# Kernel optimization log

Hardware: AMD Instinct MI355X
Metric: run time of the kernel (lower is better)

The kernel has to match this reference:

```python
import jax, jax.numpy as jnp
import numpy as np

D_NODE, C, N_HEAD = 64, 8, 8
LN_EPS = 1e-5
MASK_EPS = 1e-10
INF = 1e9


def setup_inputs() -> dict:
    key = jax.random.key(0)
    ks = jax.random.split(key, 12)
    B, S, R, D = 1, 2048, 384, D_NODE
    HC = N_HEAD * C
    M_raw = jax.random.normal(ks[0], (B, S, R, D), dtype=jnp.float32)
    M_mask = (jax.random.uniform(ks[1], (B, S, R)) > 0.1).astype(jnp.float32)
    sc = 1.0 / np.sqrt(D)
    return {
        "M_raw": M_raw,
        "M_mask": M_mask,
        "ln_g": jnp.ones((D,), jnp.float32),
        "ln_b": jnp.zeros((D,), jnp.float32),
        "Wq": jax.random.normal(ks[2], (D, HC), jnp.float32) * sc,
        "Wk": jax.random.normal(ks[3], (D, C), jnp.float32) * sc,
        "Wv": jax.random.normal(ks[4], (D, C), jnp.float32) * sc,
        "Wg": jax.random.normal(ks[5], (D, HC), jnp.float32) * sc,
        "bg": jnp.ones((HC,), jnp.float32),  # gating bias init to 1
        "Wo": jax.random.normal(ks[6], (HC, D), jnp.float32) * sc,
        "bo": jnp.zeros((D,), jnp.float32),
    }


def reference(M_raw, M_mask, ln_g, ln_b, Wq, Wk, Wv, Wg, bg, Wo, bo):
    # [B,S,R,D] -> [B,R,S,D]: attend over the sequence (column) axis per residue
    M = jnp.swapaxes(M_raw, -2, -3)
    mask = jnp.swapaxes(M_mask, -1, -2)  # [B,R,S]
    # LayerNorm over d_node
    mu = jnp.mean(M, axis=-1, keepdims=True)
    var = jnp.mean(jnp.square(M - mu), axis=-1, keepdims=True)
    M = (M - mu) * jax.lax.rsqrt(var + LN_EPS) * ln_g + ln_b
    # mean-pooled query over masked sequence positions -> [B,R,D]
    q_avg = jnp.sum(M * mask[..., None], axis=-2) / (jnp.sum(mask, axis=-1)[..., None] + MASK_EPS)
    q = (q_avg @ Wq).reshape(q_avg.shape[:-1] + (N_HEAD, C)) * (C ** -0.5)  # [B,R,H,c]
    k = M @ Wk  # [B,R,S,c] (shared across heads)
    v = M @ Wv  # [B,R,S,c]
    bias = (INF * (mask - 1.0))[..., None, :]  # [B,R,1,S]
    logits = jnp.einsum("brhc,brsc->brhs", q, k) + bias
    w = jax.nn.softmax(logits, axis=-1)
    o = jnp.einsum("brhs,brsc->brhc", w, v)  # [B,R,H,c]
    # per-position sigmoid gate broadcast against the single pooled output
    g = jax.nn.sigmoid(M @ Wg + bg).reshape(M.shape[:-1] + (N_HEAD, C))  # [B,R,S,H,c]
    go = (g * o[..., None, :, :]).reshape(M.shape[:-1] + (N_HEAD * C,))  # [B,R,S,H*c]
    out = go @ Wo + bo  # [B,R,S,D]
    return M_raw + jnp.swapaxes(out, -2, -3)
```

## Files before the change

### kernel.cpp

```cpp
#include <hip/hip_runtime.h>
#include <stdint.h>


#define DEV __device__ __forceinline__

typedef __attribute__((ext_vector_type(8))) short short8;
typedef __attribute__((ext_vector_type(4))) float floatx4;

static constexpr int S_DIM = 2048;
static constexpr int R_DIM = 384;

static constexpr size_t KV_OFF    = 0;
static constexpr size_t STATS_OFF = 25165824;
static constexpr size_t QPART_OFF = 31457280;
static constexpr size_t O_OFF     = 32342016;

DEV float bf2f(uint32_t u) { union { uint32_t i; float f; } c; c.i = u << 16; return c.f; }
DEV uint16_t f2bf(float f) {
  union { float f; uint32_t i; } c; c.f = f;
  return (uint16_t)((c.i + 0x7FFFu + ((c.i >> 16) & 1u)) >> 16);
}
DEV void unpack8(uint4 w, float* x) {
  x[0] = bf2f(w.x & 0xffff); x[1] = bf2f(w.x >> 16);
  x[2] = bf2f(w.y & 0xffff); x[3] = bf2f(w.y >> 16);
  x[4] = bf2f(w.z & 0xffff); x[5] = bf2f(w.z >> 16);
  x[6] = bf2f(w.w & 0xffff); x[7] = bf2f(w.w >> 16);
}

__global__ __launch_bounds__(256) void k1_ln_kv(
    const float* __restrict__ M, const float* __restrict__ mask,
    const float* __restrict__ lng, const float* __restrict__ lnb,
    const float* __restrict__ Wk, const float* __restrict__ Wv,
    uint16_t* __restrict__ kv, float* __restrict__ stats, float* __restrict__ qpart)
{
  __shared__ uint16_t mlnL[256 * 72];
  __shared__ uint16_t WkvT[16 * 72];
  __shared__ uint16_t kvL[256 * 16];
  __shared__ float redq[4][64];
  __shared__ float redc[4];

  const int tid = threadIdx.x;
  const int r = blockIdx.y;
  const int s_base = blockIdx.x * 256;
  const int w = tid >> 6, lane = tid & 63;
  const int g = lane >> 4, c4 = lane & 15;

#pragma unroll
  for (int i = 0; i < 4; ++i) {
    const int e = i * 256 + tid;
    const int n = e >> 6, d = e & 63;
    const float val = (n < 8) ? Wk[d * 8 + n] : Wv[d * 8 + (n - 8)];
    WkvT[n * 72 + d] = f2bf(val);
  }
  const float4 lngv = ((const float4*)lng)[c4];
  const float4 lnbv = ((const float4*)lnb)[c4];

  float qacc[4] = {0.f, 0.f, 0.f, 0.f};
  float cacc = 0.f;

#pragma unroll
  for (int j = 0; j < 16; ++j) {
    const int row_local = w * 64 + j * 4 + g;
    const int s = s_base + row_local;
    const size_t grow = (size_t)s * R_DIM + r;
    const float4 x = ((const float4*)(M + grow * 64))[c4];
    float sum = x.x + x.y + x.z + x.w;
    float ss = x.x * x.x + x.y * x.y + x.z * x.z + x.w * x.w;
#pragma unroll
    for (int off = 1; off < 16; off <<= 1) {
      sum += __shfl_xor(sum, off, 64);
      ss  += __shfl_xor(ss, off, 64);
    }
    const float mu = sum * (1.f / 64.f);
    const float var = ss * (1.f / 64.f) - mu * mu;
    const float rstd = 1.f / sqrtf(var + 1e-5f);
    if (c4 == 0) ((float2*)stats)[(size_t)r * S_DIM + s] = make_float2(mu, rstd);
    float y[4];
    y[0] = (x.x - mu) * rstd * lngv.x + lnbv.x;
    y[1] = (x.y - mu) * rstd * lngv.y + lnbv.y;
    y[2] = (x.z - mu) * rstd * lngv.z + lnbv.z;
    y[3] = (x.w - mu) * rstd * lngv.w + lnbv.w;
    uint2 p;
    p.x = (uint32_t)f2bf(y[0]) | ((uint32_t)f2bf(y[1]) << 16);
    p.y = (uint32_t)f2bf(y[2]) | ((uint32_t)f2bf(y[3]) << 16);
    *(uint2*)&mlnL[row_local * 72 + c4 * 4] = p;
    const float mval = mask[grow];
    qacc[0] += mval * y[0]; qacc[1] += mval * y[1];
    qacc[2] += mval * y[2]; qacc[3] += mval * y[3];
    cacc += mval;
  }

#pragma unroll
  for (int off = 16; off < 64; off <<= 1) {
#pragma unroll
    for (int i = 0; i < 4; ++i) qacc[i] += __shfl_xor(qacc[i], off, 64);
  }
#pragma unroll
  for (int off = 1; off < 64; off <<= 1) cacc += __shfl_xor(cacc, off, 64);
  if (lane < 16) {
    float4 qv = make_float4(qacc[0], qacc[1], qacc[2], qacc[3]);
    *(float4*)&redq[w][c4 * 4] = qv;
  }
  if (lane == 0) redc[w] = cacc * (1.f / 16.f);
  __syncthreads();

  const short8 b0 = *(const short8*)&WkvT[c4 * 72 + g * 8];
  const short8 b1 = *(const short8*)&WkvT[c4 * 72 + 32 + g * 8];
#pragma unroll
  for (int mt = 0; mt < 4; ++mt) {
    const int brow = w * 64 + mt * 16;
    const short8 a0 = *(const short8*)&mlnL[(brow + c4) * 72 + g * 8];
    const short8 a1 = *(const short8*)&mlnL[(brow + c4) * 72 + 32 + g * 8];
    floatx4 c = {0.f, 0.f, 0.f, 0.f};
    c = __builtin_amdgcn_mfma_f32_16x16x32_bf16(a0, b0, c, 0, 0, 0);
    c = __builtin_amdgcn_mfma_f32_16x16x32_bf16(a1, b1, c, 0, 0, 0);
#pragma unroll
    for (int i = 0; i < 4; ++i)
      kvL[(brow + g * 4 + i) * 16 + c4] = f2bf(c[i]);
  }
  __syncthreads();

#pragma unroll
  for (int jj = 0; jj < 4; ++jj) {
    const int row_local = w * 64 + jj * 16 + (lane >> 2);
    const int s = s_base + row_local;
    const uint2 val = *(const uint2*)&kvL[row_local * 16 + (lane & 3) * 4];
    *(uint2*)(kv + ((size_t)r * S_DIM + s) * 16 + (lane & 3) * 4) = val;
  }
  if (tid < 64)
    qpart[((size_t)r * 8 + blockIdx.x) * 72 + tid] =
        redq[0][tid] + redq[1][tid] + redq[2][tid] + redq[3][tid];
  if (tid == 64)
    qpart[((size_t)r * 8 + blockIdx.x) * 72 + 64] = redc[0] + redc[1] + redc[2] + redc[3];
}

__global__ __launch_bounds__(256) void k2_attn(
    const float* __restrict__ Wq, const float* __restrict__ mask,
    const uint16_t* __restrict__ kv, const float* __restrict__ qpart,
    float* __restrict__ oG)
{
  __shared__ float qavgL[64], qLs[64];
  __shared__ float redmax[4][8], redden[4][8], redo[4][64];
  __shared__ float cntL;
  const int tid = threadIdx.x;
  const int r = blockIdx.x;
  const int lane = tid & 63, wv = tid >> 6;

  float qs = 0.f;
  if (tid < 65) {
#pragma unroll
    for (int c = 0; c < 8; ++c) qs += qpart[((size_t)r * 8 + c) * 72 + tid];
    if (tid == 64) cntL = qs;
  }
  __syncthreads();
  if (tid < 64) qavgL[tid] = qs / (cntL + 1e-10f);
  __syncthreads();
  if (tid < 64) {
    float a = 0.f;
    for (int d = 0; d < 64; ++d) a += qavgL[d] * Wq[d * 64 + tid];
    qLs[tid] = a * 0.35355339059327373f;
  }
  __syncthreads();

  float l[64];
  float lm[8];
#pragma unroll
  for (int h = 0; h < 8; ++h) lm[h] = -3.0e38f;
  const uint4* kvp = (const uint4*)kv;
#pragma unroll
  for (int it = 0; it < 8; ++it) {
    const int s = it * 256 + tid;
    uint4 kw = kvp[((size_t)r * S_DIM + s) * 2];
    float k[8]; unpack8(kw, k);
    const float bias = (mask[(size_t)s * R_DIM + r] - 1.f) * 1e9f;
#pragma unroll
    for (int h = 0; h < 8; ++h) {
      float t = bias;
#pragma unroll
      for (int c = 0; c < 8; ++c) t += qLs[h * 8 + c] * k[c];
      l[it * 8 + h] = t;
      lm[h] = fmaxf(lm[h], t);
    }
  }
#pragma unroll
  for (int h = 0; h < 8; ++h)
#pragma unroll
    for (int off = 1; off < 64; off <<= 1) lm[h] = fmaxf(lm[h], __shfl_xor(lm[h], off, 64));
  if (lane == 0) {
#pragma unroll
    for (int h = 0; h < 8; ++h) redmax[wv][h] = lm[h];
  }
  __syncthreads();
  float gm[8];
#pragma unroll
  for (int h = 0; h < 8; ++h)
    gm[h] = fmaxf(fmaxf(redmax[0][h], redmax[1][h]), fmaxf(redmax[2][h], redmax[3][h]));

  float den[8], ao[64];
#pragma unroll
  for (int h = 0; h < 8; ++h) den[h] = 0.f;
#pragma unroll
  for (int i = 0; i < 64; ++i) ao[i] = 0.f;
#pragma unroll
  for (int it = 0; it < 8; ++it) {
    const int s = it * 256 + tid;
    uint4 vw = kvp[((size_t)r * S_DIM + s) * 2 + 1];
    float v[8]; unpack8(vw, v);
#pragma unroll
    for (int h = 0; h < 8; ++h) {
      const float w = __expf(l[it * 8 + h] - gm[h]);
      den[h] += w;
#pragma unroll
      for (int c = 0; c < 8; ++c) ao[h * 8 + c] += w * v[c];
    }
  }
#pragma unroll
  for (int st = 5; st >= 0; --st) {
    const int dist = 1 << st;
    const bool hi = (lane & dist) != 0;
#pragma unroll
    for (int j = 0; j < (1 << st); ++j) {
      const float send = hi ? ao[j] : ao[j + dist];
      const float recv = __shfl_xor(send, dist, 64);
      ao[j] = (hi ? ao[j + dist] : ao[j]) + recv;
    }
  }
#pragma unroll
  for (int h = 0; h < 8; ++h)
#pragma unroll
    for (int off = 1; off < 64; off <<= 1) den[h] += __shfl_xor(den[h], off, 64);

  redo[wv][lane] = ao[0];
  if (lane == 0) {
#pragma unroll
    for (int h = 0; h < 8; ++h) redden[wv][h] = den[h];
  }
  __syncthreads();
  if (tid < 64) {
    const float o = redo[0][tid] + redo[1][tid] + redo[2][tid] + redo[3][tid];
    const int h = tid >> 3;
    const float dd = redden[0][h] + redden[1][h] + redden[2][h] + redden[3][h];
    oG[(size_t)r * 64 + tid] = o / dd;
  }
}

__global__ __launch_bounds__(256, 2) void k3_out(
    const float* __restrict__ M, const float* __restrict__ stats,
    const float* __restrict__ oG,
    const float* __restrict__ Wg, const float* __restrict__ bg,
    const float* __restrict__ Wo, const float* __restrict__ bo,
    const float* __restrict__ lng, const float* __restrict__ lnb,
    float* __restrict__ out)
{
  __shared__ uint16_t mlnL[256 * 72];
  __shared__ uint16_t WgT[64 * 72];
  __shared__ uint16_t WoT[64 * 72];
  __shared__ float oLs[64];
  const int tid = threadIdx.x;
  const int r = blockIdx.y;
  const int s_base = blockIdx.x * 256;
  const int w = tid >> 6, lane = tid & 63;
  const int g = lane >> 4, c4 = lane & 15;

#pragma unroll
  for (int i = 0; i < 16; ++i) {
    const int idx = i * 256 + tid;
    const int a = idx >> 6, b = idx & 63;
    WgT[b * 72 + a] = f2bf(Wg[idx]);
    WoT[b * 72 + a] = f2bf(Wo[idx]);
  }
  if (tid < 64) oLs[tid] = oG[(size_t)r * 64 + tid];
  const float4 lngv = ((const float4*)lng)[c4];
  const float4 lnbv = ((const float4*)lnb)[c4];

#pragma unroll
  for (int j = 0; j < 16; ++j) {
    const int row_local = w * 64 + j * 4 + g;
    const int s = s_base + row_local;
    const size_t grow = (size_t)s * R_DIM + r;
    const float2 st = ((const float2*)stats)[(size_t)r * S_DIM + s];
    const float4 x = ((const float4*)(M + grow * 64))[c4];
    float y[4];
    y[0] = (x.x - st.x) * st.y * lngv.x + lnbv.x;
    y[1] = (x.y - st.x) * st.y * lngv.y + lnbv.y;
    y[2] = (x.z - st.x) * st.y * lngv.z + lnbv.z;
    y[3] = (x.w - st.x) * st.y * lngv.w + lnbv.w;
    uint2 p;
    p.x = (uint32_t)f2bf(y[0]) | ((uint32_t)f2bf(y[1]) << 16);
    p.y = (uint32_t)f2bf(y[2]) | ((uint32_t)f2bf(y[3]) << 16);
    *(uint2*)&mlnL[row_local * 72 + c4 * 4] = p;
  }
  __syncthreads();

  const int wrow0 = w * 64;
  const int mrow = c4;
  const int quad = g;

  short8 wgB[4][2], woB[4][2];
#pragma unroll
  for (int nt = 0; nt < 4; ++nt)
#pragma unroll
    for (int kk = 0; kk < 2; ++kk) {
      wgB[nt][kk] = *(const short8*)(&WgT[(nt * 16 + mrow) * 72 + kk * 32 + quad * 8]);
      woB[nt][kk] = *(const short8*)(&WoT[(nt * 16 + mrow) * 72 + kk * 32 + quad * 8]);
    }
  float og[4], bgr[4], bor[4];
#pragma unroll
  for (int nt = 0; nt < 4; ++nt) {
    og[nt] = oLs[nt * 16 + mrow];
    bgr[nt] = bg[nt * 16 + mrow];
    bor[nt] = bo[nt * 16 + mrow];
  }

#pragma unroll
  for (int mt = 0; mt < 4; ++mt) {
    const int arow = (wrow0 + mt * 16 + mrow) * 72 + quad * 8;
    const short8 a0 = *(const short8*)(&mlnL[arow]);
    const short8 a1 = *(const short8*)(&mlnL[arow + 32]);
#pragma unroll
    for (int nt = 0; nt < 4; ++nt) {
      floatx4 c = {0.f, 0.f, 0.f, 0.f};
      c = __builtin_amdgcn_mfma_f32_16x16x32_bf16(a0, wgB[nt][0], c, 0, 0, 0);
      c = __builtin_amdgcn_mfma_f32_16x16x32_bf16(a1, wgB[nt][1], c, 0, 0, 0);
#pragma unroll
      for (int i = 0; i < 4; ++i) {
        const float z = c[i] + bgr[nt];
        const float gt = 1.0f / (1.0f + __expf(-z));
        mlnL[(wrow0 + mt * 16 + quad * 4 + i) * 72 + nt * 16 + mrow] = f2bf(gt * og[nt]);
      }
    }
  }
  __syncthreads();

#pragma unroll
  for (int mt = 0; mt < 4; ++mt) {
    const int arow = (wrow0 + mt * 16 + mrow) * 72 + quad * 8;
    const short8 a0 = *(const short8*)(&mlnL[arow]);
    const short8 a1 = *(const short8*)(&mlnL[arow + 32]);
#pragma unroll
    for (int nt = 0; nt < 4; ++nt) {
      floatx4 c = {0.f, 0.f, 0.f, 0.f};
      c = __builtin_amdgcn_mfma_f32_16x16x32_bf16(a0, woB[nt][0], c, 0, 0, 0);
      c = __builtin_amdgcn_mfma_f32_16x16x32_bf16(a1, woB[nt][1], c, 0, 0, 0);
#pragma unroll
      for (int i = 0; i < 4; ++i)
        mlnL[(wrow0 + mt * 16 + quad * 4 + i) * 72 + nt * 16 + mrow] = f2bf(c[i] + bor[nt]);
    }
  }
  __syncthreads();

#pragma unroll
  for (int j = 0; j < 16; ++j) {
    const int row_local = w * 64 + j * 4 + g;
    const int s = s_base + row_local;
    const size_t grow = (size_t)s * R_DIM + r;
    const float4 x = ((const float4*)(M + grow * 64))[c4];
    const uint2 tv = *(const uint2*)&mlnL[row_local * 72 + c4 * 4];
    float4 o;
    o.x = x.x + bf2f(tv.x & 0xffff);
    o.y = x.y + bf2f(tv.x >> 16);
    o.z = x.z + bf2f(tv.y & 0xffff);
    o.w = x.w + bf2f(tv.y >> 16);
    ((float4*)(out + grow * 64))[c4] = o;
  }
}

extern "C" void kernel_launch(void* const* d_in, const int* in_sizes, int n_in,
                              void* d_out, int out_size, void* d_ws, size_t ws_size,
                              hipStream_t stream)
{
  const float* M    = (const float*)d_in[0];
  const float* mask = (const float*)d_in[1];
  const float* lng  = (const float*)d_in[2];
  const float* lnb  = (const float*)d_in[3];
  const float* Wq   = (const float*)d_in[4];
  const float* Wk   = (const float*)d_in[5];
  const float* Wv   = (const float*)d_in[6];
  const float* Wg   = (const float*)d_in[7];
  const float* bg   = (const float*)d_in[8];
  const float* Wo   = (const float*)d_in[9];
  const float* bo   = (const float*)d_in[10];
  float* out = (float*)d_out;

  char* ws = (char*)d_ws;
  uint16_t* kvB  = (uint16_t*)(ws + KV_OFF);
  float* statsB  = (float*)(ws + STATS_OFF);
  float* qpartB  = (float*)(ws + QPART_OFF);
  float* oB      = (float*)(ws + O_OFF);

  k1_ln_kv<<<dim3(8, 384), 256, 0, stream>>>(M, mask, lng, lnb, Wk, Wv, kvB, statsB, qpartB);
  k2_attn<<<dim3(384), 256, 0, stream>>>(Wq, mask, kvB, qpartB, oB);
  k3_out<<<dim3(8, 384), 256, 0, stream>>>(M, statsB, oB, Wg, bg, Wo, bo, lng, lnb, out);
}
```

Measured before the change: 472.5 us.

## Retile LN/KV and output kernels for coalesced 4-residue reads, drop stats buffer

Both the LN+KV kernel and the output kernel now give each wave 4 adjacent residues times 64 sequence positions, so each 16-lane group reads a contiguous 256-byte row and the 4 residues share a 1 KB span. Previously each block handled a single residue with a 98 KB stride between rows. The stats workspace is removed and the output kernel recomputes LayerNorm, trading a little ALU work for less global traffic. Per-wave small LDS tiles replace the block-wide buffers and barriers, and q partials are now split into 32 chunks, which adds reduction work in the attention kernel.

```diff
diff --git a/kernel.cpp b/kernel.cpp
--- a/kernel.cpp
+++ b/kernel.cpp
@@ -9,11 +9,11 @@
 
 static constexpr int S_DIM = 2048;
 static constexpr int R_DIM = 384;
+static constexpr int NCH   = 32;
 
 static constexpr size_t KV_OFF    = 0;
-static constexpr size_t STATS_OFF = 25165824;
-static constexpr size_t QPART_OFF = 31457280;
-static constexpr size_t O_OFF     = 32342016;
+static constexpr size_t QPART_OFF = 25165824;
+static constexpr size_t O_OFF     = 28704768;
 
 DEV float bf2f(uint32_t u) { union { uint32_t i; float f; } c; c.i = u << 16; return c.f; }
 DEV uint16_t f2bf(float f) {
@@ -31,19 +31,18 @@
     const float* __restrict__ M, const float* __restrict__ mask,
     const float* __restrict__ lng, const float* __restrict__ lnb,
     const float* __restrict__ Wk, const float* __restrict__ Wv,
-    uint16_t* __restrict__ kv, float* __restrict__ stats, float* __restrict__ qpart)
+    uint16_t* __restrict__ kv, float* __restrict__ qpart)
 {
-  __shared__ uint16_t mlnL[256 * 72];
   __shared__ uint16_t WkvT[16 * 72];
-  __shared__ uint16_t kvL[256 * 16];
-  __shared__ float redq[4][64];
-  __shared__ float redc[4];
+  __shared__ uint16_t mlnA[4][16 * 72];
+  __shared__ uint16_t kvS[4][4 * 64 * 16];
 
   const int tid = threadIdx.x;
-  const int r = blockIdx.y;
-  const int s_base = blockIdx.x * 256;
   const int w = tid >> 6, lane = tid & 63;
-  const int g = lane >> 4, c4 = lane & 15;
+  const int rl = lane >> 4, c4 = lane & 15;
+  const int sc = blockIdx.x;
+  const int s0 = sc * 64;
+  const int r0w = blockIdx.y * 16 + w * 4;
 
 #pragma unroll
   for (int i = 0; i < 4; ++i) {
@@ -54,84 +53,77 @@
   }
   const float4 lngv = ((const float4*)lng)[c4];
   const float4 lnbv = ((const float4*)lnb)[c4];
+  __syncthreads();
+
+  const short8 b0 = *(const short8*)&WkvT[c4 * 72 + rl * 8];
+  const short8 b1 = *(const short8*)&WkvT[c4 * 72 + 32 + rl * 8];
+
+  uint16_t* mA = mlnA[w];
+  uint16_t* kS = kvS[w];
 
   float qacc[4] = {0.f, 0.f, 0.f, 0.f};
   float cacc = 0.f;
 
-#pragma unroll
-  for (int j = 0; j < 16; ++j) {
-    const int row_local = w * 64 + j * 4 + g;
-    const int s = s_base + row_local;
-    const size_t grow = (size_t)s * R_DIM + r;
-    const float4 x = ((const float4*)(M + grow * 64))[c4];
-    float sum = x.x + x.y + x.z + x.w;
-    float ss = x.x * x.x + x.y * x.y + x.z * x.z + x.w * x.w;
-#pragma unroll
-    for (int off = 1; off < 16; off <<= 1) {
-      sum += __shfl_xor(sum, off, 64);
-      ss  += __shfl_xor(ss, off, 64);
-    }
-    const float mu = sum * (1.f / 64.f);
-    const float var = ss * (1.f / 64.f) - mu * mu;
-    const float rstd = 1.f / sqrtf(var + 1e-5f);
-    if (c4 == 0) ((float2*)stats)[(size_t)r * S_DIM + s] = make_float2(mu, rstd);
-    float y[4];
-    y[0] = (x.x - mu) * rstd * lngv.x + lnbv.x;
-    y[1] = (x.y - mu) * rstd * lngv.y + lnbv.y;
-    y[2] = (x.z - mu) * rstd * lngv.z + lnbv.z;
-    y[3] = (x.w - mu) * rstd * lngv.w + lnbv.w;
-    uint2 p;
-    p.x = (uint32_t)f2bf(y[0]) | ((uint32_t)f2bf(y[1]) << 16);
-    p.y = (uint32_t)f2bf(y[2]) | ((uint32_t)f2bf(y[3]) << 16);
-    *(uint2*)&mlnL[row_local * 72 + c4 * 4] = p;
-    const float mval = mask[grow];
-    qacc[0] += mval * y[0]; qacc[1] += mval * y[1];
-    qacc[2] += mval * y[2]; qacc[3] += mval * y[3];
-    cacc += mval;
-  }
-
-#pragma unroll
-  for (int off = 16; off < 64; off <<= 1) {
-#pragma unroll
-    for (int i = 0; i < 4; ++i) qacc[i] += __shfl_xor(qacc[i], off, 64);
-  }
-#pragma unroll
-  for (int off = 1; off < 64; off <<= 1) cacc += __shfl_xor(cacc, off, 64);
-  if (lane < 16) {
-    float4 qv = make_float4(qacc[0], qacc[1], qacc[2], qacc[3]);
-    *(float4*)&redq[w][c4 * 4] = qv;
-  }
-  if (lane == 0) redc[w] = cacc * (1.f / 16.f);
-  __syncthreads();
-
-  const short8 b0 = *(const short8*)&WkvT[c4 * 72 + g * 8];
-  const short8 b1 = *(const short8*)&WkvT[c4 * 72 + 32 + g * 8];
-#pragma unroll
-  for (int mt = 0; mt < 4; ++mt) {
-    const int brow = w * 64 + mt * 16;
-    const short8 a0 = *(const short8*)&mlnL[(brow + c4) * 72 + g * 8];
-    const short8 a1 = *(const short8*)&mlnL[(brow + c4) * 72 + 32 + g * 8];
+#pragma unroll 2
+  for (int grp = 0; grp < 16; ++grp) {
+    const int sg = s0 + grp * 4;
+    float4 xg[4];
+    float mv[4];
+#pragma unroll
+    for (int si = 0; si < 4; ++si) {
+      const size_t grow = (size_t)(sg + si) * R_DIM + r0w + rl;
+      xg[si] = ((const float4*)(M + grow * 64))[c4];
+      mv[si] = mask[grow];
+    }
+#pragma unroll
+    for (int si = 0; si < 4; ++si) {
+      const float4 x = xg[si];
+      float sum = x.x + x.y + x.z + x.w;
+      float ss = x.x * x.x + x.y * x.y + x.z * x.z + x.w * x.w;
+#pragma unroll
+      for (int off = 1; off < 16; off <<= 1) {
+        sum += __shfl_xor(sum, off, 64);
+        ss  += __shfl_xor(ss, off, 64);
+      }
+      const float mu = sum * (1.f / 64.f);
+      const float var = ss * (1.f / 64.f) - mu * mu;
+      const float rstd = 1.f / sqrtf(var + 1e-5f);
+      float y[4];
+      y[0] = (x.x - mu) * rstd * lngv.x + lnbv.x;
+      y[1] = (x.y - mu) * rstd * lngv.y + lnbv.y;
+      y[2] = (x.z - mu) * rstd * lngv.z + lnbv.z;
+      y[3] = (x.w - mu) * rstd * lngv.w + lnbv.w;
+      uint2 p;
+      p.x = (uint32_t)f2bf(y[0]) | ((uint32_t)f2bf(y[1]) << 16);
+      p.y = (uint32_t)f2bf(y[2]) | ((uint32_t)f2bf(y[3]) << 16);
+      *(uint2*)&mA[(si * 4 + rl) * 72 + c4 * 4] = p;
+      const float m = mv[si];
+      qacc[0] += m * y[0]; qacc[1] += m * y[1];
+      qacc[2] += m * y[2]; qacc[3] += m * y[3];
+      cacc += m;
+    }
+    const short8 a0 = *(const short8*)&mA[c4 * 72 + rl * 8];
+    const short8 a1 = *(const short8*)&mA[c4 * 72 + 32 + rl * 8];
     floatx4 c = {0.f, 0.f, 0.f, 0.f};
     c = __builtin_amdgcn_mfma_f32_16x16x32_bf16(a0, b0, c, 0, 0, 0);
     c = __builtin_amdgcn_mfma_f32_16x16x32_bf16(a1, b1, c, 0, 0, 0);
 #pragma unroll
     for (int i = 0; i < 4; ++i)
-      kvL[(brow + g * 4 + i) * 16 + c4] = f2bf(c[i]);
-  }
-  __syncthreads();
-
-#pragma unroll
-  for (int jj = 0; jj < 4; ++jj) {
-    const int row_local = w * 64 + jj * 16 + (lane >> 2);
-    const int s = s_base + row_local;
-    const uint2 val = *(const uint2*)&kvL[row_local * 16 + (lane & 3) * 4];
-    *(uint2*)(kv + ((size_t)r * S_DIM + s) * 16 + (lane & 3) * 4) = val;
-  }
-  if (tid < 64)
-    qpart[((size_t)r * 8 + blockIdx.x) * 72 + tid] =
-        redq[0][tid] + redq[1][tid] + redq[2][tid] + redq[3][tid];
-  if (tid == 64)
-    qpart[((size_t)r * 8 + blockIdx.x) * 72 + 64] = redc[0] + redc[1] + redc[2] + redc[3];
+      kS[i * 1024 + (grp * 4 + rl) * 16 + c4] = f2bf(c[i]);
+  }
+
+#pragma unroll
+  for (int i = 0; i < 4; ++i) {
+#pragma unroll
+    for (int t = 0; t < 2; ++t) {
+      const uint4 val = *(const uint4*)&kS[i * 1024 + t * 512 + lane * 8];
+      *(uint4*)(kv + ((size_t)(r0w + i) * S_DIM + s0) * 16 + t * 512 + lane * 8) = val;
+    }
+  }
+  *(float4*)&qpart[((size_t)(r0w + rl) * NCH + sc) * 72 + c4 * 4] =
+      make_float4(qacc[0], qacc[1], qacc[2], qacc[3]);
+  if (c4 == 0)
+    qpart[((size_t)(r0w + rl) * NCH + sc) * 72 + 64] = cacc;
 }
 
 __global__ __launch_bounds__(256) void k2_attn(
@@ -149,7 +141,7 @@
   float qs = 0.f;
   if (tid < 65) {
 #pragma unroll
-    for (int c = 0; c < 8; ++c) qs += qpart[((size_t)r * 8 + c) * 72 + tid];
+    for (int c = 0; c < NCH; ++c) qs += qpart[((size_t)r * NCH + c) * 72 + tid];
     if (tid == 64) cntL = qs;
   }
   __syncthreads();
@@ -245,22 +237,23 @@
 }
 
 __global__ __launch_bounds__(256, 2) void k3_out(
-    const float* __restrict__ M, const float* __restrict__ stats,
-    const float* __restrict__ oG,
+    const float* __restrict__ M, const float* __restrict__ oG,
     const float* __restrict__ Wg, const float* __restrict__ bg,
     const float* __restrict__ Wo, const float* __restrict__ bo,
     const float* __restrict__ lng, const float* __restrict__ lnb,
     float* __restrict__ out)
 {
-  __shared__ uint16_t mlnL[256 * 72];
   __shared__ uint16_t WgT[64 * 72];
   __shared__ uint16_t WoT[64 * 72];
-  __shared__ float oLs[64];
+  __shared__ uint16_t mlnA[4][16 * 72];
+  __shared__ uint16_t tA[4][16 * 72];
+
   const int tid = threadIdx.x;
-  const int r = blockIdx.y;
-  const int s_base = blockIdx.x * 256;
   const int w = tid >> 6, lane = tid & 63;
-  const int g = lane >> 4, c4 = lane & 15;
+  const int rl = lane >> 4, c4 = lane & 15;
+  const int sc = blockIdx.x;
+  const int s0 = sc * 64;
+  const int r0w = blockIdx.y * 16 + w * 4;
 
 #pragma unroll
   for (int i = 0; i < 16; ++i) {
@@ -269,99 +262,103 @@
     WgT[b * 72 + a] = f2bf(Wg[idx]);
     WoT[b * 72 + a] = f2bf(Wo[idx]);
   }
-  if (tid < 64) oLs[tid] = oG[(size_t)r * 64 + tid];
   const float4 lngv = ((const float4*)lng)[c4];
   const float4 lnbv = ((const float4*)lnb)[c4];
-
-#pragma unroll
-  for (int j = 0; j < 16; ++j) {
-    const int row_local = w * 64 + j * 4 + g;
-    const int s = s_base + row_local;
-    const size_t grow = (size_t)s * R_DIM + r;
-    const float2 st = ((const float2*)stats)[(size_t)r * S_DIM + s];
-    const float4 x = ((const float4*)(M + grow * 64))[c4];
-    float y[4];
-    y[0] = (x.x - st.x) * st.y * lngv.x + lnbv.x;
-    y[1] = (x.y - st.x) * st.y * lngv.y + lnbv.y;
-    y[2] = (x.z - st.x) * st.y * lngv.z + lnbv.z;
-    y[3] = (x.w - st.x) * st.y * lngv.w + lnbv.w;
-    uint2 p;
-    p.x = (uint32_t)f2bf(y[0]) | ((uint32_t)f2bf(y[1]) << 16);
-    p.y = (uint32_t)f2bf(y[2]) | ((uint32_t)f2bf(y[3]) << 16);
-    *(uint2*)&mlnL[row_local * 72 + c4 * 4] = p;
-  }
-  __syncthreads();
-
-  const int wrow0 = w * 64;
-  const int mrow = c4;
-  const int quad = g;
+  __syncthreads();
 
   short8 wgB[4][2], woB[4][2];
 #pragma unroll
   for (int nt = 0; nt < 4; ++nt)
 #pragma unroll
     for (int kk = 0; kk < 2; ++kk) {
-      wgB[nt][kk] = *(const short8*)(&WgT[(nt * 16 + mrow) * 72 + kk * 32 + quad * 8]);
-      woB[nt][kk] = *(const short8*)(&WoT[(nt * 16 + mrow) * 72 + kk * 32 + quad * 8]);
-    }
-  float og[4], bgr[4], bor[4];
+      wgB[nt][kk] = *(const short8*)&WgT[(nt * 16 + c4) * 72 + kk * 32 + rl * 8];
+      woB[nt][kk] = *(const short8*)&WoT[(nt * 16 + c4) * 72 + kk * 32 + rl * 8];
+    }
+  float og[4][4], bgr[4], bor[4];
 #pragma unroll
   for (int nt = 0; nt < 4; ++nt) {
-    og[nt] = oLs[nt * 16 + mrow];
-    bgr[nt] = bg[nt * 16 + mrow];
-    bor[nt] = bo[nt * 16 + mrow];
-  }
-
-#pragma unroll
-  for (int mt = 0; mt < 4; ++mt) {
-    const int arow = (wrow0 + mt * 16 + mrow) * 72 + quad * 8;
-    const short8 a0 = *(const short8*)(&mlnL[arow]);
-    const short8 a1 = *(const short8*)(&mlnL[arow + 32]);
-#pragma unroll
-    for (int nt = 0; nt < 4; ++nt) {
-      floatx4 c = {0.f, 0.f, 0.f, 0.f};
-      c = __builtin_amdgcn_mfma_f32_16x16x32_bf16(a0, wgB[nt][0], c, 0, 0, 0);
-      c = __builtin_amdgcn_mfma_f32_16x16x32_bf16(a1, wgB[nt][1], c, 0, 0, 0);
-#pragma unroll
-      for (int i = 0; i < 4; ++i) {
-        const float z = c[i] + bgr[nt];
-        const float gt = 1.0f / (1.0f + __expf(-z));
-        mlnL[(wrow0 + mt * 16 + quad * 4 + i) * 72 + nt * 16 + mrow] = f2bf(gt * og[nt]);
+    bgr[nt] = bg[nt * 16 + c4];
+    bor[nt] = bo[nt * 16 + c4];
+#pragma unroll
+    for (int i = 0; i < 4; ++i)
+      og[nt][i] = oG[(size_t)(r0w + i) * 64 + nt * 16 + c4];
+  }
+
+  uint16_t* mA = mlnA[w];
+  uint16_t* tAw = tA[w];
+
+#pragma unroll 2
+  for (int grp = 0; grp < 16; ++grp) {
+    const int sg = s0 + grp * 4;
+    float4 xg[4];
+#pragma unroll
+    for (int si = 0; si < 4; ++si)
+      xg[si] = ((const float4*)(M + ((size_t)(sg + si) * R_DIM + r0w + rl) * 64))[c4];
+
+#pragma unroll
+    for (int si = 0; si < 4; ++si) {
+      const float4 x = xg[si];
+      float sum = x.x + x.y + x.z + x.w;
+      float ss = x.x * x.x + x.y * x.y + x.z * x.z + x.w * x.w;
+#pragma unroll
+      for (int off = 1; off < 16; off <<= 1) {
+        sum += __shfl_xor(sum, off, 64);
+        ss  += __shfl_xor(ss, off, 64);
       }
-    }
-  }
-  __syncthreads();
-
-#pragma unroll
-  for (int mt = 0; mt < 4; ++mt) {
-    const int arow = (wrow0 + mt * 16 + mrow) * 72 + quad * 8;
-    const short8 a0 = *(const short8*)(&mlnL[arow]);
-    const short8 a1 = *(const short8*)(&mlnL[arow + 32]);
-#pragma unroll
-    for (int nt = 0; nt < 4; ++nt) {
-      floatx4 c = {0.f, 0.f, 0.f, 0.f};
-      c = __builtin_amdgcn_mfma_f32_16x16x32_bf16(a0, woB[nt][0], c, 0, 0, 0);
-      c = __builtin_amdgcn_mfma_f32_16x16x32_bf16(a1, woB[nt][1], c, 0, 0, 0);
-#pragma unroll
-      for (int i = 0; i < 4; ++i)
-        mlnL[(wrow0 + mt * 16 + quad * 4 + i) * 72 + nt * 16 + mrow] = f2bf(c[i] + bor[nt]);
-    }
-  }
-  __syncthreads();
-
-#pragma unroll
-  for (int j = 0; j < 16; ++j) {
-    const int row_local = w * 64 + j * 4 + g;
-    const int s = s_base + row_local;
-    const size_t grow = (size_t)s * R_DIM + r;
-    const float4 x = ((const float4*)(M + grow * 64))[c4];
-    const uint2 tv = *(const uint2*)&mlnL[row_local * 72 + c4 * 4];
-    float4 o;
-    o.x = x.x + bf2f(tv.x & 0xffff);
-    o.y = x.y + bf2f(tv.x >> 16);
-    o.z = x.z + bf2f(tv.y & 0xffff);
-    o.w = x.w + bf2f(tv.y >> 16);
-    ((float4*)(out + grow * 64))[c4] = o;
+      const float mu = sum * (1.f / 64.f);
+      const float var = ss * (1.f / 64.f) - mu * mu;
+      const float rstd = 1.f / sqrtf(var + 1e-5f);
+      float y[4];
+      y[0] = (x.x - mu) * rstd * lngv.x + lnbv.x;
+      y[1] = (x.y - mu) * rstd * lngv.y + lnbv.y;
+      y[2] = (x.z - mu) * rstd * lngv.z + lnbv.z;
+      y[3] = (x.w - mu) * rstd * lngv.w + lnbv.w;
+      uint2 p;
+      p.x = (uint32_t)f2bf(y[0]) | ((uint32_t)f2bf(y[1]) << 16);
+      p.y = (uint32_t)f2bf(y[2]) | ((uint32_t)f2bf(y[3]) << 16);
+      *(uint2*)&mA[(si * 4 + rl) * 72 + c4 * 4] = p;
+    }
+
+    {
+      const short8 a0 = *(const short8*)&mA[c4 * 72 + rl * 8];
+      const short8 a1 = *(const short8*)&mA[c4 * 72 + 32 + rl * 8];
+#pragma unroll
+      for (int nt = 0; nt < 4; ++nt) {
+        floatx4 c = {0.f, 0.f, 0.f, 0.f};
+        c = __builtin_amdgcn_mfma_f32_16x16x32_bf16(a0, wgB[nt][0], c, 0, 0, 0);
+        c = __builtin_amdgcn_mfma_f32_16x16x32_bf16(a1, wgB[nt][1], c, 0, 0, 0);
+#pragma unroll
+        for (int i = 0; i < 4; ++i) {
+          const float z = c[i] + bgr[nt];
+          const float gt = 1.0f / (1.0f + __expf(-z));
+          tAw[(rl * 4 + i) * 72 + nt * 16 + c4] = f2bf(gt * og[nt][i]);
+        }
+      }
+    }
+    {
+      const short8 a0 = *(const short8*)&tAw[c4 * 72 + rl * 8];
+      const short8 a1 = *(const short8*)&tAw[c4 * 72 + 32 + rl * 8];
+#pragma unroll
+      for (int nt = 0; nt < 4; ++nt) {
+        floatx4 c = {0.f, 0.f, 0.f, 0.f};
+        c = __builtin_amdgcn_mfma_f32_16x16x32_bf16(a0, woB[nt][0], c, 0, 0, 0);
+        c = __builtin_amdgcn_mfma_f32_16x16x32_bf16(a1, woB[nt][1], c, 0, 0, 0);
+#pragma unroll
+        for (int i = 0; i < 4; ++i)
+          mA[(rl * 4 + i) * 72 + nt * 16 + c4] = f2bf(c[i] + bor[nt]);
+      }
+    }
+#pragma unroll
+    for (int si = 0; si < 4; ++si) {
+      const uint2 tv = *(const uint2*)&mA[(si * 4 + rl) * 72 + c4 * 4];
+      const float4 x = xg[si];
+      float4 o;
+      o.x = x.x + bf2f(tv.x & 0xffff);
+      o.y = x.y + bf2f(tv.x >> 16);
+      o.z = x.z + bf2f(tv.y & 0xffff);
+      o.w = x.w + bf2f(tv.y >> 16);
+      ((float4*)(out + ((size_t)(sg + si) * R_DIM + r0w + rl) * 64))[c4] = o;
+    }
   }
 }
 
@@ -384,11 +381,10 @@
 
   char* ws = (char*)d_ws;
   uint16_t* kvB  = (uint16_t*)(ws + KV_OFF);
-  float* statsB  = (float*)(ws + STATS_OFF);
   float* qpartB  = (float*)(ws + QPART_OFF);
   float* oB      = (float*)(ws + O_OFF);
 
-  k1_ln_kv<<<dim3(8, 384), 256, 0, stream>>>(M, mask, lng, lnb, Wk, Wv, kvB, statsB, qpartB);
-  k2_attn<<<dim3(384), 256, 0, stream>>>(Wq, mask, kvB, qpartB, oB);
-  k3_out<<<dim3(8, 384), 256, 0, stream>>>(M, statsB, oB, Wg, bg, Wo, bo, lng, lnb, out);
-}
+  k1_ln_kv<<<dim3(NCH, 24), 256, 0, stream>>>(M, mask, lng, lnb, Wk, Wv, kvB, qpartB);
+  k2_attn<<<dim3(R_DIM), 256, 0, stream>>>(Wq, mask, kvB, qpartB, oB);
+  k3_out<<<dim3(NCH, 24), 256, 0, stream>>>(M, oB, Wg, bg, Wo, bo, lng, lnb, out);
+}
```

Result: faster. 457.6 us (-3.2%).
